# Kernel tuning notes

Measured on AMD Instinct MI355X. Metric: run time of the kernel, lower is better.

The kernel has to match this reference:

```python
import jax, jax.numpy as jnp
import numpy as np

N = 1024   # nnodes
H = 8      # attention heads
C = 32     # gnn_repr_size (per head)
HC = H * C # 256
E = 65536  # num edges
ER = 32    # edge_repr_size
F = 3      # feat_emb_size
NUM_STOPS = 512


def setup_inputs() -> dict:
    key = jax.random.key(0)
    ks = jax.random.split(key, 24)
    g = lambda i, shape, s: jax.random.normal(ks[i], shape, dtype=jnp.float32) * s
    return {
        "dist": jax.random.uniform(ks[0], (N, N), dtype=jnp.float32),
        "stops": jax.random.randint(ks[1], (NUM_STOPS,), 0, N),
        "weekday": 3,
        "vehicles": 5,
        "markov": jax.random.uniform(ks[2], (N, N), dtype=jnp.float32),
        "demand": jax.random.uniform(ks[3], (N, 1), dtype=jnp.float32),
        "capacity": 10,
        "edge_index": jax.random.randint(ks[4], (2, E), 0, N),
        # GATConv layer 1 (in=1, out=H*C, edge_dim=1)
        "W1": g(5, (1, HC), 1.0), "We1": g(6, (1, HC), 1.0),
        "a_src1": g(7, (H, C), 0.1), "a_dst1": g(8, (H, C), 0.1), "a_edge1": g(9, (H, C), 0.1),
        "b1": jnp.zeros((HC,), jnp.float32),
        # GATConv layer 2 (in=H*C, out=H*C)
        "W2": g(10, (HC, HC), 0.0625), "We2": g(11, (1, HC), 1.0),
        "a_src2": g(12, (H, C), 0.1), "a_dst2": g(13, (H, C), 0.1), "a_edge2": g(14, (H, C), 0.1),
        "b2": jnp.zeros((HC,), jnp.float32),
        # edge summarizer Linear(2*HC, ER)
        "Wes": g(15, (2 * HC, ER), 0.0442), "bes": jnp.zeros((ER,), jnp.float32),
        # scalar embeddings
        "emb_weekday": g(16, (7, F), 0.1), "emb_capacity": g(17, (26, F), 0.1), "emb_vehicle": g(18, (15, F), 0.1),
        # combiner MLP: Linear(N*ER + 3N + 3F, N), Linear(N, N)
        "Wc1": g(19, (N * ER + 3 * N + 3 * F, N), 0.0053), "bc1": jnp.zeros((N,), jnp.float32),
        "Wc2": g(20, (N, N), 0.03125), "bc2": jnp.zeros((N,), jnp.float32),
    }


def _gat(x, src, dst, edge_attr, W, We, a_src, a_dst, a_edge, b):
    """PyG GATConv (concat heads, eval mode so attention dropout is identity)."""
    h = (x @ W).reshape(-1, H, C)                   # [N, H, C]
    e = (edge_attr @ We).reshape(-1, H, C)          # [E, H, C]
    alpha = (h * a_src).sum(-1)[src] + (h * a_dst).sum(-1)[dst] + (e * a_edge).sum(-1)  # [E, H]
    alpha = jax.nn.leaky_relu(alpha, 0.2)
    # segment softmax over destination nodes
    m = jax.ops.segment_max(alpha, dst, num_segments=N)
    m = jnp.where(jnp.isfinite(m), m, 0.0)
    ex = jnp.exp(alpha - m[dst])
    denom = jax.ops.segment_sum(ex, dst, num_segments=N)
    coef = ex / (denom[dst] + 1e-16)                # [E, H]
    out = jax.ops.segment_sum(h[src] * coef[:, :, None], dst, num_segments=N)  # [N, H, C]
    return out.reshape(-1, HC) + b


def reference(dist, stops, weekday, vehicles, markov, demand, capacity, edge_index,
              W1, We1, a_src1, a_dst1, a_edge1, b1,
              W2, We2, a_src2, a_dst2, a_edge2, b2,
              Wes, bes, emb_weekday, emb_capacity, emb_vehicle,
              Wc1, bc1, Wc2, bc2):
    src, dst = edge_index[0], edge_index[1]
    dist = (dist - dist.min()) / (dist.max() - dist.min())
    edge_attr = markov[src, dst][:, None]           # [E, 1]
    x = _gat(demand, src, dst, edge_attr, W1, We1, a_src1, a_dst1, a_edge1, b1)
    x = jax.nn.relu(x)
    x = _gat(x, src, dst, edge_attr, W2, We2, a_src2, a_dst2, a_edge2, b2)
    x = jax.nn.relu(x)                              # [N, HC]
    # edge_summarizer(cat(x_i, x_j)) decomposed: x_i @ Wes_top + x_j @ Wes_bot + bes
    ea = x @ Wes[:HC]                               # [N, ER]
    eb = x @ Wes[HC:]                               # [N, ER]
    edge_repr = (ea[:, None, :] + eb[None, :, :] + bes).reshape(N, N * ER)
    wf = jnp.broadcast_to(emb_weekday[weekday][None, :], (N, F))
    cf = jnp.broadcast_to(emb_capacity[capacity][None, :], (N, F))
    vf = jnp.broadcast_to(emb_vehicle[vehicles][None, :], (N, F))
    sf = jnp.zeros((N,), jnp.float32).at[stops].set(1.0)
    sf = jnp.broadcast_to(sf[None, :], (N, N))
    combined = jnp.concatenate([edge_repr, dist, markov, wf, cf, vf, sf], axis=1)
    out = jax.nn.relu(combined @ Wc1 + bc1) @ Wc2 + bc2  # [N, N]
    return out
```

## Files before the change

### kernel.cpp

```cpp
#include <hip/hip_runtime.h>

#define NN 1024
#define NE 65536

typedef short v8s __attribute__((ext_vector_type(8)));
typedef float v4f __attribute__((ext_vector_type(4)));

constexpr size_t OF_SCAL = 0;
constexpr size_t OF_MMP  = 64;
constexpr size_t OF_DEG  = 1088;
constexpr size_t OF_OFF  = 2112;
constexpr size_t OF_CUR  = 3200;
constexpr size_t OF_EIDX = 4224;
constexpr size_t OF_MARK = 69760;
constexpr size_t OF_X1H  = 135296;
constexpr size_t OF_X1L  = 266368;
constexpr size_t OF_H2   = 397440;
constexpr size_t OF_S2S  = 659584;
constexpr size_t OF_S2D  = 667776;
constexpr size_t OF_DEN2 = 675968;
constexpr size_t OF_EX2  = 684160;
constexpr size_t OF_X2   = 1208448;
constexpr size_t OF_BCAT = 1470592;
constexpr size_t OF_EAB  = 1486976;
constexpr size_t OF_WVEC = 1552512;
constexpr size_t OF_SRP  = 1588608;
constexpr size_t OF_C0P  = 3685760;
constexpr size_t OF_SR   = 3759488;
constexpr size_t OF_BASE = 3792256;
constexpr size_t OF_AH   = 3793280;
constexpr size_t OF_AL   = 4858240;
constexpr size_t OF_BTH  = 5923200;
constexpr size_t OF_BTL  = 6988160;
constexpr size_t OF_HH   = 8053120;
constexpr size_t OF_HL   = 8577408;
constexpr size_t OF_W2TH = 9101696;
constexpr size_t OF_W2TL = 9134464;
constexpr size_t OF_WC2TH= 9167232;
constexpr size_t OF_WC2TL= 9691520;
constexpr size_t OF_P0   = 10215808;

__device__ inline unsigned short f2bf(float x){
  unsigned u = __float_as_uint(x);
  unsigned r = u + 0x7fffu + ((u>>16)&1u);
  return (unsigned short)(r>>16);
}
__device__ inline float bf2f(unsigned short h){
  return __uint_as_float(((unsigned)h)<<16);
}

__global__ void k_mm1(const float* __restrict__ dist, float* mnP, float* mxP, int* __restrict__ deg){
  __shared__ float smn[256], smx[256];
  int tid = threadIdx.x;
  if (blockIdx.x < 4) deg[blockIdx.x*256 + tid] = 0;
  float mn = 1e30f, mx = -1e30f;
  for (int i = blockIdx.x*256 + tid; i < NN*NN; i += gridDim.x*256){
    float v = dist[i]; mn = fminf(mn, v); mx = fmaxf(mx, v);
  }
  smn[tid]=mn; smx[tid]=mx; __syncthreads();
  for (int s=128; s>0; s>>=1){
    if (tid<s){ smn[tid]=fminf(smn[tid],smn[tid+s]); smx[tid]=fmaxf(smx[tid],smx[tid+s]); }
    __syncthreads();
  }
  if (tid==0){ mnP[blockIdx.x]=smn[0]; mxP[blockIdx.x]=smx[0]; }
}

__global__ __launch_bounds__(512) void k_misc(const float* mnP, const float* mxP, float* scal,
    const float* W1, const float* We1, const float* as1, const float* ad1, const float* ae1,
    const float* We2, const float* ae2,
    const float* ew, const float* ec, const float* ev,
    const int* wd, const int* cap, const int* veh, const int* stops, float* wvec,
    const float* Wes, float* Bcat){
  int b = blockIdx.x, t = threadIdx.x;
  if (b == 0){
    __shared__ float smn[512], smx[512];
    smn[t]=mnP[t]; smx[t]=mxP[t]; __syncthreads();
    for (int s=256; s>0; s>>=1){
      if (t<s){ smn[t]=fminf(smn[t],smn[t+s]); smx[t]=fmaxf(smx[t],smx[t+s]); }
      __syncthreads();
    }
    if (t==0){ scal[0]=smn[0]; scal[1]=1.0f/(smx[0]-smn[0]); }
  } else if (b == 1){
    if (t < 8){
      float s=0.f, d=0.f, e=0.f, e2=0.f;
      for (int c=0;c<32;c++){
        int i = t*32+c;
        s += W1[i]*as1[i]; d += W1[i]*ad1[i]; e += We1[i]*ae1[i]; e2 += We2[i]*ae2[i];
      }
      scal[16+t]=s; scal[24+t]=d; scal[32+t]=e; scal[40+t]=e2;
    }
  } else if (b == 2){
    for (int m = 32768 + t; m < 35904; m += 512){
      float v = 0.f;
      if (m >= 34816 && m < 34819) v = ew[wd[0]*3 + (m-34816)];
      else if (m >= 34819 && m < 34822) v = ec[cap[0]*3 + (m-34819)];
      else if (m >= 34822 && m < 34825) v = ev[veh[0]*3 + (m-34822)];
      wvec[m] = v;
    }
    __syncthreads();
    wvec[34825 + stops[t]] = 1.0f;
  } else {
    int idx = (b-3)*512 + t;
    int k = idx >> 6, r = idx & 63;
    Bcat[idx] = (r < 32) ? Wes[(size_t)k*32 + r] : Wes[(size_t)(256+k)*32 + (r-32)];
  }
}

__global__ void k_edges(const int* __restrict__ ei, const float* __restrict__ markov,
                        float* __restrict__ mark, int* __restrict__ deg){
  int e = blockIdx.x*256 + threadIdx.x;
  if (e >= NE) return;
  int s = ei[e], d = ei[NE+e];
  mark[e] = markov[(size_t)s*NN + d];
  atomicAdd(&deg[d], 1);
}

__global__ void k_scan(const int* deg, int* off, int* cur){
  __shared__ int tmp[NN];
  int t = threadIdx.x;
  tmp[t] = deg[t]; __syncthreads();
  for (int s=1; s<NN; s<<=1){
    int v = (t>=s) ? tmp[t-s] : 0;
    __syncthreads();
    tmp[t] += v;
    __syncthreads();
  }
  int ex = (t==0) ? 0 : tmp[t-1];
  off[t]=ex; cur[t]=ex;
  if (t==NN-1) off[NN]=tmp[NN-1];
}

__global__ void k_fill(const int* __restrict__ ei, int* __restrict__ cur, int* __restrict__ eidxl){
  int e = blockIdx.x*256 + threadIdx.x;
  if (e >= NE) return;
  int d = ei[NE+e];
  int p = atomicAdd(&cur[d], 1);
  eidxl[p] = e;
}

__global__ __launch_bounds__(64) void k_gat1x1(const int* __restrict__ ei, const int* __restrict__ eidxl,
    const int* __restrict__ off, const float* __restrict__ mark, const float* __restrict__ demand,
    const float* __restrict__ scal, const float* __restrict__ W1, const float* __restrict__ b1,
    unsigned short* __restrict__ X1h, unsigned short* __restrict__ X1l){
  int n = blockIdx.x, lane = threadIdx.x;
  int o0 = off[n], o1 = off[n+1];
  float dn = demand[n];
  float cs[8], cd[8], ce[8], mx[8];
  #pragma unroll
  for (int h=0;h<8;h++){ cs[h]=scal[16+h]; cd[h]=scal[24+h]; ce[h]=scal[32+h]; mx[h]=-1e30f; }
  for (int i=o0+lane; i<o1; i+=64){
    int e = eidxl[i]; float ds = demand[ei[e]]; float me = mark[e];
    #pragma unroll
    for (int h=0;h<8;h++){
      float a = ds*cs[h] + dn*cd[h] + me*ce[h];
      a = a < 0.f ? 0.2f*a : a;
      mx[h] = fmaxf(mx[h], a);
    }
  }
  #pragma unroll
  for (int s=32; s>0; s>>=1){
    #pragma unroll
    for (int h=0;h<8;h++) mx[h] = fmaxf(mx[h], __shfl_xor(mx[h], s));
  }
  float se[8], sd_[8];
  #pragma unroll
  for (int h=0;h<8;h++){ se[h]=0.f; sd_[h]=0.f; }
  for (int i=o0+lane; i<o1; i+=64){
    int e = eidxl[i]; float ds = demand[ei[e]]; float me = mark[e];
    #pragma unroll
    for (int h=0;h<8;h++){
      float a = ds*cs[h] + dn*cd[h] + me*ce[h];
      a = a < 0.f ? 0.2f*a : a;
      float ex = expf(a - mx[h]);
      se[h] += ex; sd_[h] += ex*ds;
    }
  }
  #pragma unroll
  for (int s=32; s>0; s>>=1){
    #pragma unroll
    for (int h=0;h<8;h++){ se[h] += __shfl_xor(se[h], s); sd_[h] += __shfl_xor(sd_[h], s); }
  }
  float t1v[8];
  #pragma unroll
  for (int h=0;h<8;h++) t1v[h] = sd_[h] / (se[h] + 1e-16f);
  #pragma unroll
  for (int q=0;q<4;q++){
    int hc = lane + q*64; int h = hc >> 5;
    float v = fmaxf(t1v[h]*W1[hc] + b1[hc], 0.f);
    unsigned short hh = f2bf(v);
    X1h[(size_t)n*256 + hc] = hh;
    X1l[(size_t)n*256 + hc] = f2bf(v - bf2f(hh));
  }
}

__global__ __launch_bounds__(256) void gemm64(const float* __restrict__ A, int lda,
    const float* __restrict__ B, int ldb, float* __restrict__ C, int ldc, int K,
    const float* __restrict__ bias, int dorelu){
  __shared__ float As[16][68];
  __shared__ float Bs[16][68];
  int tid = threadIdx.x;
  int tx = tid & 15, ty = tid >> 4;
  int row0 = ty*4, col0 = tx*4;
  int gm = blockIdx.y*64, gn = blockIdx.x*64;
  float acc[4][4] = {};
  for (int k0 = 0; k0 < K; k0 += 16){
    #pragma unroll
    for (int q=0;q<4;q++){
      int idx = tid*4+q; int i = idx>>4, kk = idx&15;
      As[kk][i] = A[(size_t)(gm+i)*lda + k0 + kk];
    }
    #pragma unroll
    for (int q=0;q<4;q++){
      int idx = tid*4+q; int kk = idx>>6, j = idx&63;
      Bs[kk][j] = B[(size_t)(k0+kk)*ldb + gn + j];
    }
    __syncthreads();
    #pragma unroll
    for (int kk=0;kk<16;kk++){
      float a0=As[kk][row0+0], a1=As[kk][row0+1], a2=As[kk][row0+2], a3=As[kk][row0+3];
      float b0=Bs[kk][col0+0], b1=Bs[kk][col0+1], b2=Bs[kk][col0+2], b3=Bs[kk][col0+3];
      acc[0][0]+=a0*b0; acc[0][1]+=a0*b1; acc[0][2]+=a0*b2; acc[0][3]+=a0*b3;
      acc[1][0]+=a1*b0; acc[1][1]+=a1*b1; acc[1][2]+=a1*b2; acc[1][3]+=a1*b3;
      acc[2][0]+=a2*b0; acc[2][1]+=a2*b1; acc[2][2]+=a2*b2; acc[2][3]+=a2*b3;
      acc[3][0]+=a3*b0; acc[3][1]+=a3*b1; acc[3][2]+=a3*b2; acc[3][3]+=a3*b3;
    }
    __syncthreads();
  }
  #pragma unroll
  for (int i=0;i<4;i++){
    #pragma unroll
    for (int j=0;j<4;j++){
      int cc = gn + col0 + j;
      float v = acc[i][j];
      if (bias) v += bias[cc];
      if (dorelu) v = fmaxf(v, 0.f);
      C[(size_t)(gm+row0+i)*ldc + cc] = v;
    }
  }
}

__global__ void k_s2(const float* __restrict__ h2, const float* __restrict__ as2,
                     const float* __restrict__ ad2, float* __restrict__ s2s, float* __restrict__ s2d){
  int idx = blockIdx.x*256 + threadIdx.x;
  if (idx >= NN*8) return;
  int n = idx >> 3, h = idx & 7;
  float ss = 0.f, sd = 0.f;
  for (int c=0;c<32;c++){
    float v = h2[(size_t)n*256 + h*32 + c];
    ss += v*as2[h*32+c]; sd += v*ad2[h*32+c];
  }
  s2s[idx]=ss; s2d[idx]=sd;
}

__global__ __launch_bounds__(64) void k_gat2maxex(const int* __restrict__ ei, const int* __restrict__ eidxl,
    const int* __restrict__ off, const float* __restrict__ mark, const float* __restrict__ s2s,
    const float* __restrict__ s2d, const float* __restrict__ scal,
    float* __restrict__ den, float* __restrict__ ex2){
  int n = blockIdx.x, lane = threadIdx.x;
  int o0 = off[n], o1 = off[n+1];
  float ce[8], sdn[8], mx[8];
  #pragma unroll
  for (int h=0;h<8;h++){ ce[h]=scal[40+h]; sdn[h]=s2d[n*8+h]; mx[h]=-1e30f; }
  for (int i=o0+lane; i<o1; i+=64){
    int e = eidxl[i]; int s = ei[e]; float me = mark[e];
    #pragma unroll
    for (int h=0;h<8;h++){
      float a = s2s[s*8+h] + sdn[h] + me*ce[h];
      a = a < 0.f ? 0.2f*a : a;
      mx[h] = fmaxf(mx[h], a);
    }
  }
  #pragma unroll
  for (int sft=32; sft>0; sft>>=1){
    #pragma unroll
    for (int h=0;h<8;h++) mx[h] = fmaxf(mx[h], __shfl_xor(mx[h], sft));
  }
  float se[8];
  #pragma unroll
  for (int h=0;h<8;h++) se[h]=0.f;
  for (int i=o0+lane; i<o1; i+=64){
    int e = eidxl[i]; int s = ei[e]; float me = mark[e];
    float exv[8];
    #pragma unroll
    for (int h=0;h<8;h++){
      float a = s2s[s*8+h] + sdn[h] + me*ce[h];
      a = a < 0.f ? 0.2f*a : a;
      exv[h] = expf(a - mx[h]);
      se[h] += exv[h];
    }
    #pragma unroll
    for (int h=0;h<8;h++) ex2[(size_t)e*8+h] = exv[h];
  }
  #pragma unroll
  for (int sft=32; sft>0; sft>>=1){
    #pragma unroll
    for (int h=0;h<8;h++) se[h] += __shfl_xor(se[h], sft);
  }
  if (lane==0){
    #pragma unroll
    for (int h=0;h<8;h++) den[n*8+h] = se[h];
  }
}

__global__ __launch_bounds__(256) void k_agg2(const int* __restrict__ ei, const int* __restrict__ eidxl,
    const int* __restrict__ off, const float* __restrict__ ex2, const float* __restrict__ den,
    const float* __restrict__ h2, const float* __restrict__ b2, float* __restrict__ x2){
  __shared__ int eL[64], sL[64];
  __shared__ float cf[64*8];
  int n = blockIdx.x, tid = threadIdx.x, h = tid >> 5;
  int o0 = off[n], o1 = off[n+1];
  float inv = 1.0f/(den[n*8+h] + 1e-16f);
  float acc = 0.f;
  for (int b = o0; b < o1; b += 64){
    int len = min(64, o1 - b);
    __syncthreads();
    if (tid < len){ int e = eidxl[b+tid]; eL[tid]=e; sL[tid]=ei[e]; }
    __syncthreads();
    for (int idx = tid; idx < len*8; idx += 256)
      cf[idx] = ex2[(size_t)eL[idx>>3]*8 + (idx&7)];
    __syncthreads();
    for (int j=0;j<len;j++){
      acc += cf[j*8 + h] * h2[(size_t)sL[j]*256 + tid];
    }
  }
  x2[(size_t)n*256 + tid] = fmaxf(acc*inv + b2[tid], 0.f);
}

__global__ void k_wvec(const float* __restrict__ eab, const float* __restrict__ bes,
                       float* __restrict__ wvec){
  int m = blockIdx.x*256 + threadIdx.x;
  int j = m >> 5, r = m & 31;
  wvec[m] = eab[(size_t)j*64 + 32 + r] + bes[r];
}

__global__ __launch_bounds__(256) void k_src0(const float* __restrict__ Wc1, const float* __restrict__ wvec,
                                              float* __restrict__ srP, float* __restrict__ c0P){
  __shared__ float c0s[256*4];
  int t = threadIdx.x;
  int kg = t & 31;
  int rg = t >> 5;
  int col = blockIdx.x*128 + kg*4;
  int chunk = blockIdx.y;
  int m0 = chunk*512;
  float sr[4][4];
  #pragma unroll
  for (int u=0;u<4;u++){ sr[u][0]=0.f; sr[u][1]=0.f; sr[u][2]=0.f; sr[u][3]=0.f; }
  float c0a[4] = {0.f,0.f,0.f,0.f};
  for (int jj=0; jj<16; ++jj){
    int rbase = m0 + jj*32 + rg*4;
    #pragma unroll
    for (int u=0;u<4;u++){
      int m = rbase + u;
      float4 w = make_float4(0.f,0.f,0.f,0.f);
      float wv = 0.f;
      if (m < 35849){
        w = *reinterpret_cast<const float4*>(&Wc1[(size_t)m*1024 + col]);
        wv = wvec[m];
      }
      c0a[0] += wv*w.x; c0a[1] += wv*w.y; c0a[2] += wv*w.z; c0a[3] += wv*w.w;
      if (chunk < 64){
        sr[u][0] += w.x; sr[u][1] += w.y; sr[u][2] += w.z; sr[u][3] += w.w;
      }
    }
  }
  if (chunk < 64){
    #pragma unroll
    for (int u=0;u<4;u++){
      int r = rg*4 + u;
      float4 v = make_float4(sr[u][0], sr[u][1], sr[u][2], sr[u][3]);
      *reinterpret_cast<float4*>(&srP[(size_t)(chunk*32 + r)*1024 + col]) = v;
    }
  }
  c0s[t*4+0]=c0a[0]; c0s[t*4+1]=c0a[1]; c0s[t*4+2]=c0a[2]; c0s[t*4+3]=c0a[3];
  __syncthreads();
  if (t < 32){
    float s0=0.f,s1=0.f,s2=0.f,s3=0.f;
    #pragma unroll
    for (int q=0;q<8;q++){
      int b = (t + q*32)*4;
      s0 += c0s[b+0]; s1 += c0s[b+1]; s2 += c0s[b+2]; s3 += c0s[b+3];
    }
    float4 v = make_float4(s0,s1,s2,s3);
    *reinterpret_cast<float4*>(&c0P[(size_t)chunk*1024 + blockIdx.x*128 + t*4]) = v;
  }
}

__global__ void k_stage2(const float* __restrict__ srP, const float* __restrict__ c0P,
                         const float* __restrict__ bc1, float* __restrict__ Sr, float* __restrict__ base){
  int idx = blockIdx.x*256 + threadIdx.x;
  if (idx < 8192){
    int r = idx >> 8, k4 = idx & 255;
    float s0=0.f,s1=0.f,s2=0.f,s3=0.f;
    for (int c=0;c<64;c++){
      float4 v = *reinterpret_cast<const float4*>(&srP[(size_t)(c*32 + r)*1024 + k4*4]);
      s0+=v.x; s1+=v.y; s2+=v.z; s3+=v.w;
    }
    float4 o = make_float4(s0,s1,s2,s3);
    *reinterpret_cast<float4*>(&Sr[(size_t)r*1024 + k4*4]) = o;
  } else if (idx < 8448){
    int k4 = idx - 8192;
    float4 b = *reinterpret_cast<const float4*>(&bc1[k4*4]);
    float s0=b.x, s1=b.y, s2=b.z, s3=b.w;
    for (int c=0;c<71;c++){
      float4 v = *reinterpret_cast<const float4*>(&c0P[(size_t)c*1024 + k4*4]);
      s0+=v.x; s1+=v.y; s2+=v.z; s3+=v.w;
    }
    float4 o = make_float4(s0,s1,s2,s3);
    *reinterpret_cast<float4*>(&base[k4*4]) = o;
  }
}

__global__ void k_cvtA(const float* __restrict__ dist, const float* __restrict__ markov,
                       const float* __restrict__ eab, const float* __restrict__ scal,
                       unsigned short* __restrict__ Ah, unsigned short* __restrict__ Al){
  int k = blockIdx.x*256 + threadIdx.x;
  int i = blockIdx.y;
  if (k >= 2080) return;
  float mn = scal[0], inv = scal[1];
  float v;
  if (k < 1024) v = (dist[(size_t)i*1024 + k] - mn)*inv;
  else if (k < 2048) v = markov[(size_t)i*1024 + (k-1024)];
  else v = eab[(size_t)i*64 + (k-2048)];
  unsigned short h = f2bf(v);
  Ah[(size_t)i*2080 + k] = h;
  Al[(size_t)i*2080 + k] = f2bf(v - bf2f(h));
}

__global__ void k_cvtT(const float* __restrict__ src, const float* __restrict__ src2, int k2,
                       int lds, int ldt, unsigned short* __restrict__ Th, unsigned short* __restrict__ Tl){
  __shared__ unsigned short shh[32][65], shl[32][65];
  int t = threadIdx.x;
  int k0 = blockIdx.x*32, n0 = blockIdx.y*64;
  #pragma unroll
  for (int q=0;q<8;q++){
    int idx = t + q*256;
    int kl = idx >> 6, nl = idx & 63;
    int k = k0 + kl;
    float v = (k < k2) ? src[(size_t)k*lds + n0 + nl] : src2[(size_t)(k-k2)*lds + n0 + nl];
    unsigned short h = f2bf(v);
    shh[kl][nl] = h;
    shl[kl][nl] = f2bf(v - bf2f(h));
  }
  __syncthreads();
  #pragma unroll
  for (int q=0;q<8;q++){
    int idx = t + q*256;
    int nl = idx >> 5, kl = idx & 31;
    Th[(size_t)(n0+nl)*ldt + k0 + kl] = shh[kl][nl];
    Tl[(size_t)(n0+nl)*ldt + k0 + kl] = shl[kl][nl];
  }
}

__global__ __launch_bounds__(256) void k_mfma128(
    const unsigned short* __restrict__ Ah, const unsigned short* __restrict__ Al, int lda,
    const unsigned short* __restrict__ Bth, const unsigned short* __restrict__ Btl, int ldb,
    float* __restrict__ Cp, int ldc, int kSteps, int kTot){
  __shared__ __align__(16) unsigned short Ash[128*32], Asl[128*32], Bsh[128*32], Bsl[128*32];
  int t = threadIdx.x;
  int wave = t >> 6, lane = t & 63;
  int wr = wave >> 1, wc = wave & 1;
  int gm = blockIdx.y*128, gn = blockIdx.x*128;
  float* plane = Cp + ((size_t)blockIdx.z << 20);
  int ks0 = blockIdx.z * kSteps;
  int ks1 = ks0 + kSteps; if (ks1 > kTot) ks1 = kTot;

  int kq = lane >> 4;
  int l15 = lane & 15;
  int r0s = t >> 2,        s0s = t & 3;
  int r1s = (t+256) >> 2,  s1s = t & 3;

  v4f acc[4][4];
  #pragma unroll
  for (int i=0;i<4;i++)
    #pragma unroll
    for (int j=0;j<4;j++) acc[i][j] = (v4f){0.f,0.f,0.f,0.f};

  for (int ks = ks0; ks < ks1; ++ks){
    int kb = ks*32;
    const size_t a0 = (size_t)(gm+r0s)*lda + kb + s0s*8;
    const size_t a1 = (size_t)(gm+r1s)*lda + kb + s1s*8;
    const size_t b0 = (size_t)(gn+r0s)*ldb + kb + s0s*8;
    const size_t b1 = (size_t)(gn+r1s)*ldb + kb + s1s*8;
    v8s gah0 = *(const v8s*)(Ah + a0), gah1 = *(const v8s*)(Ah + a1);
    v8s gal0 = *(const v8s*)(Al + a0), gal1 = *(const v8s*)(Al + a1);
    v8s gbh0 = *(const v8s*)(Bth + b0), gbh1 = *(const v8s*)(Bth + b1);
    v8s gbl0 = *(const v8s*)(Btl + b0), gbl1 = *(const v8s*)(Btl + b1);
    __syncthreads();
    int w0 = r0s*32 + ((s0s ^ ((r0s>>1)&3))*8);
    int w1 = r1s*32 + ((s1s ^ ((r1s>>1)&3))*8);
    *(v8s*)(Ash + w0) = gah0;  *(v8s*)(Ash + w1) = gah1;
    *(v8s*)(Asl + w0) = gal0;  *(v8s*)(Asl + w1) = gal1;
    *(v8s*)(Bsh + w0) = gbh0;  *(v8s*)(Bsh + w1) = gbh1;
    *(v8s*)(Bsl + w0) = gbl0;  *(v8s*)(Bsl + w1) = gbl1;
    __syncthreads();
    v8s fbh[4], fbl[4];
    #pragma unroll
    for (int fj=0; fj<4; fj++){
      int cb = wc*64 + fj*16 + l15;
      int boff = cb*32 + ((kq ^ ((cb>>1)&3))*8);
      fbh[fj] = *(v8s*)(Bsh + boff);
      fbl[fj] = *(v8s*)(Bsl + boff);
    }
    #pragma unroll
    for (int fi=0; fi<4; fi++){
      int ra = wr*64 + fi*16 + l15;
      int aoff = ra*32 + ((kq ^ ((ra>>1)&3))*8);
      v8s fah = *(v8s*)(Ash + aoff);
      v8s fal = *(v8s*)(Asl + aoff);
      #pragma unroll
      for (int fj=0; fj<4; fj++){
        acc[fi][fj] = __builtin_amdgcn_mfma_f32_16x16x32_bf16(fah, fbh[fj], acc[fi][fj], 0, 0, 0);
        acc[fi][fj] = __builtin_amdgcn_mfma_f32_16x16x32_bf16(fah, fbl[fj], acc[fi][fj], 0, 0, 0);
        acc[fi][fj] = __builtin_amdgcn_mfma_f32_16x16x32_bf16(fal, fbh[fj], acc[fi][fj], 0, 0, 0);
      }
    }
  }
  int row0 = gm + wr*64 + (lane>>4)*4;
  int col0 = gn + wc*64 + l15;
  #pragma unroll
  for (int fi=0; fi<4; fi++)
    #pragma unroll
    for (int fj=0; fj<4; fj++)
      #pragma unroll
      for (int r=0; r<4; r++)
        plane[(size_t)(row0 + fi*16 + r)*ldc + col0 + fj*16] = acc[fi][fj][r];
}

__global__ void k_fin2(const float* __restrict__ P, float* __restrict__ h2){
  int idx = blockIdx.x*256 + threadIdx.x;
  float4 a = *reinterpret_cast<const float4*>(P + (size_t)idx*4);
  float4 b = *reinterpret_cast<const float4*>(P + (1u<<20) + (size_t)idx*4);
  float4 o = make_float4(a.x+b.x, a.y+b.y, a.z+b.z, a.w+b.w);
  *reinterpret_cast<float4*>(h2 + (size_t)idx*4) = o;
}

__global__ void k_fin_hidden(const float* __restrict__ P, const float* __restrict__ base,
                             unsigned short* __restrict__ Hh, unsigned short* __restrict__ Hl){
  int idx = blockIdx.x*256 + threadIdx.x;
  float4 s = *reinterpret_cast<const float4*>(base + ((idx & 255)*4));
  #pragma unroll
  for (int p=0;p<8;p++){
    float4 v = *reinterpret_cast<const float4*>(P + ((size_t)p<<20) + (size_t)idx*4);
    s.x+=v.x; s.y+=v.y; s.z+=v.z; s.w+=v.w;
  }
  float vv[4] = {s.x, s.y, s.z, s.w};
  unsigned short hh[4], hl[4];
  #pragma unroll
  for (int q=0;q<4;q++){
    float x = fmaxf(vv[q], 0.f);
    hh[q] = f2bf(x);
    hl[q] = f2bf(x - bf2f(hh[q]));
  }
  *reinterpret_cast<uint2*>(Hh + (size_t)idx*4) = *reinterpret_cast<uint2*>(hh);
  *reinterpret_cast<uint2*>(Hl + (size_t)idx*4) = *reinterpret_cast<uint2*>(hl);
}

__global__ void k_fin_out(const float* __restrict__ P, const float* __restrict__ bc2,
                          float* __restrict__ out){
  int idx = blockIdx.x*256 + threadIdx.x;
  float4 s = *reinterpret_cast<const float4*>(bc2 + ((idx & 255)*4));
  #pragma unroll
  for (int p=0;p<8;p++){
    float4 v = *reinterpret_cast<const float4*>(P + ((size_t)p<<20) + (size_t)idx*4);
    s.x+=v.x; s.y+=v.y; s.z+=v.z; s.w+=v.w;
  }
  *reinterpret_cast<float4*>(out + (size_t)idx*4) = s;
}

extern "C" void kernel_launch(void* const* d_in, const int* in_sizes, int n_in,
                              void* d_out, int out_size, void* d_ws, size_t ws_size,
                              hipStream_t stream){
  const float* dist     = (const float*)d_in[0];
  const int*   stops    = (const int*)  d_in[1];
  const int*   weekday  = (const int*)  d_in[2];
  const int*   vehicles = (const int*)  d_in[3];
  const float* markov   = (const float*)d_in[4];
  const float* demand   = (const float*)d_in[5];
  const int*   capacity = (const int*)  d_in[6];
  const int*   ei       = (const int*)  d_in[7];
  const float* W1  = (const float*)d_in[8];
  const float* We1 = (const float*)d_in[9];
  const float* as1 = (const float*)d_in[10];
  const float* ad1 = (const float*)d_in[11];
  const float* ae1 = (const float*)d_in[12];
  const float* b1  = (const float*)d_in[13];
  const float* W2  = (const float*)d_in[14];
  const float* We2 = (const float*)d_in[15];
  const float* as2 = (const float*)d_in[16];
  const float* ad2 = (const float*)d_in[17];
  const float* ae2 = (const float*)d_in[18];
  const float* b2  = (const float*)d_in[19];
  const float* Wes = (const float*)d_in[20];
  const float* bes = (const float*)d_in[21];
  const float* ew  = (const float*)d_in[22];
  const float* ec  = (const float*)d_in[23];
  const float* ev  = (const float*)d_in[24];
  const float* Wc1 = (const float*)d_in[25];
  const float* bc1 = (const float*)d_in[26];
  const float* Wc2 = (const float*)d_in[27];
  const float* bc2 = (const float*)d_in[28];

  float* W    = (float*)d_ws;
  float* scal = W + OF_SCAL;
  float* mmP  = W + OF_MMP;
  int*   deg  = (int*)(W + OF_DEG);
  int*   off  = (int*)(W + OF_OFF);
  int*   cur  = (int*)(W + OF_CUR);
  int*   eidxl= (int*)(W + OF_EIDX);
  float* mark = W + OF_MARK;
  unsigned short* X1h = (unsigned short*)(W + OF_X1H);
  unsigned short* X1l = (unsigned short*)(W + OF_X1L);
  float* h2   = W + OF_H2;
  float* s2s  = W + OF_S2S;
  float* s2d  = W + OF_S2D;
  float* den2 = W + OF_DEN2;
  float* ex2  = W + OF_EX2;
  float* x2   = W + OF_X2;
  float* Bcat = W + OF_BCAT;
  float* eab  = W + OF_EAB;
  float* wvec = W + OF_WVEC;
  float* srP  = W + OF_SRP;
  float* c0P  = W + OF_C0P;
  float* Sr   = W + OF_SR;
  float* base = W + OF_BASE;
  unsigned short* Ah    = (unsigned short*)(W + OF_AH);
  unsigned short* Al    = (unsigned short*)(W + OF_AL);
  unsigned short* Bth   = (unsigned short*)(W + OF_BTH);
  unsigned short* Btl   = (unsigned short*)(W + OF_BTL);
  unsigned short* Hh    = (unsigned short*)(W + OF_HH);
  unsigned short* Hl    = (unsigned short*)(W + OF_HL);
  unsigned short* W2th  = (unsigned short*)(W + OF_W2TH);
  unsigned short* W2tl  = (unsigned short*)(W + OF_W2TL);
  unsigned short* Wc2th = (unsigned short*)(W + OF_WC2TH);
  unsigned short* Wc2tl = (unsigned short*)(W + OF_WC2TL);
  float* P0   = W + OF_P0;
  float* out  = (float*)d_out;

  k_mm1 <<<dim3(512), dim3(256), 0, stream>>>(dist, mmP, mmP+512, deg);
  k_misc<<<dim3(35), dim3(512), 0, stream>>>(mmP, mmP+512, scal, W1, We1, as1, ad1, ae1, We2, ae2,
                                             ew, ec, ev, weekday, capacity, vehicles, stops, wvec, Wes, Bcat);
  k_cvtT<<<dim3(8,4), dim3(256), 0, stream>>>(W2, W2, 1<<30, 256, 256, W2th, W2tl);
  k_cvtT<<<dim3(32,16), dim3(256), 0, stream>>>(Wc2, Wc2, 1<<30, 1024, 1024, Wc2th, Wc2tl);
  k_edges<<<dim3(256), dim3(256), 0, stream>>>(ei, markov, mark, deg);
  k_scan<<<dim3(1), dim3(1024), 0, stream>>>(deg, off, cur);
  k_fill<<<dim3(256), dim3(256), 0, stream>>>(ei, cur, eidxl);
  k_gat1x1<<<dim3(1024), dim3(64), 0, stream>>>(ei, eidxl, off, mark, demand, scal, W1, b1, X1h, X1l);
  k_mfma128<<<dim3(2,8,2), dim3(256), 0, stream>>>(X1h, X1l, 256, W2th, W2tl, 256, P0, 256, 4, 8);
  k_fin2<<<dim3(256), dim3(256), 0, stream>>>(P0, h2);
  k_s2  <<<dim3(32), dim3(256), 0, stream>>>(h2, as2, ad2, s2s, s2d);
  k_gat2maxex<<<dim3(1024), dim3(64), 0, stream>>>(ei, eidxl, off, mark, s2s, s2d, scal, den2, ex2);
  k_agg2<<<dim3(1024), dim3(256), 0, stream>>>(ei, eidxl, off, ex2, den2, h2, b2, x2);
  gemm64<<<dim3(1,16), dim3(256), 0, stream>>>(x2, 256, Bcat, 64, eab, 64, 256, (const float*)nullptr, 0);
  k_wvec<<<dim3(128), dim3(256), 0, stream>>>(eab, bes, wvec);
  k_src0<<<dim3(8,71), dim3(256), 0, stream>>>(Wc1, wvec, srP, c0P);
  k_stage2<<<dim3(33), dim3(256), 0, stream>>>(srP, c0P, bc1, Sr, base);
  k_cvtA<<<dim3(9,1024), dim3(256), 0, stream>>>(dist, markov, eab, scal, Ah, Al);
  k_cvtT<<<dim3(65,16), dim3(256), 0, stream>>>(Wc1 + (size_t)32768*1024, Sr, 2048, 1024, 2080, Bth, Btl);
  k_mfma128<<<dim3(8,8,8), dim3(256), 0, stream>>>(Ah, Al, 2080, Bth, Btl, 2080, P0, 1024, 9, 65);
  k_fin_hidden<<<dim3(1024), dim3(256), 0, stream>>>(P0, base, Hh, Hl);
  k_mfma128<<<dim3(8,8,8), dim3(256), 0, stream>>>(Hh, Hl, 1024, Wc2th, Wc2tl, 1024, P0, 1024, 4, 32);
  k_fin_out<<<dim3(1024), dim3(256), 0, stream>>>(P0, bc2, out);
}
```

Baseline: 201.0 us.

## Fuse small kernels and retune split-K partitioning across GEMM stages

Merges the two weight-transpose conversions into one launch, fuses the h2 split-K reduction with the per-head attention score computation, and folds the wvec bias add into the small gemm epilogue, removing several launches and round trips through global memory. It also doubles the chunk count in the Wc1 column-sum pass to expose more parallelism, and changes split-K factors: the W2 GEMM goes from 2 to 8 splits, while the large hidden and output GEMMs drop from 8 to 4 splits, with the matching reduce loops shortened. Workspace offsets are moved to fit the larger partial buffers. The trade-off is fewer parallel blocks in the big GEMMs against less partial-sum traffic.

```diff
diff --git a/kernel.cpp b/kernel.cpp
--- a/kernel.cpp
+++ b/kernel.cpp
@@ -25,20 +25,20 @@
 constexpr size_t OF_EAB  = 1486976;
 constexpr size_t OF_WVEC = 1552512;
 constexpr size_t OF_SRP  = 1588608;
-constexpr size_t OF_C0P  = 3685760;
-constexpr size_t OF_SR   = 3759488;
-constexpr size_t OF_BASE = 3792256;
-constexpr size_t OF_AH   = 3793280;
-constexpr size_t OF_AL   = 4858240;
-constexpr size_t OF_BTH  = 5923200;
-constexpr size_t OF_BTL  = 6988160;
-constexpr size_t OF_HH   = 8053120;
-constexpr size_t OF_HL   = 8577408;
-constexpr size_t OF_W2TH = 9101696;
-constexpr size_t OF_W2TL = 9134464;
-constexpr size_t OF_WC2TH= 9167232;
-constexpr size_t OF_WC2TL= 9691520;
-constexpr size_t OF_P0   = 10215808;
+constexpr size_t OF_C0P  = 5782912;
+constexpr size_t OF_SR   = 5928320;
+constexpr size_t OF_BASE = 5961088;
+constexpr size_t OF_AH   = 5962112;
+constexpr size_t OF_AL   = 7027072;
+constexpr size_t OF_BTH  = 8092032;
+constexpr size_t OF_BTL  = 9156992;
+constexpr size_t OF_HH   = 10221952;
+constexpr size_t OF_HL   = 10746240;
+constexpr size_t OF_W2TH = 11270528;
+constexpr size_t OF_W2TL = 11303296;
+constexpr size_t OF_WC2TH= 11336064;
+constexpr size_t OF_WC2TL= 11860352;
+constexpr size_t OF_P0   = 12384640;
 
 __device__ inline unsigned short f2bf(float x){
   unsigned u = __float_as_uint(x);
@@ -195,7 +195,7 @@
 
 __global__ __launch_bounds__(256) void gemm64(const float* __restrict__ A, int lda,
     const float* __restrict__ B, int ldb, float* __restrict__ C, int ldc, int K,
-    const float* __restrict__ bias, int dorelu){
+    float* __restrict__ wvec, const float* __restrict__ bes){
   __shared__ float As[16][68];
   __shared__ float Bs[16][68];
   int tid = threadIdx.x;
@@ -232,24 +232,32 @@
     for (int j=0;j<4;j++){
       int cc = gn + col0 + j;
       float v = acc[i][j];
-      if (bias) v += bias[cc];
-      if (dorelu) v = fmaxf(v, 0.f);
       C[(size_t)(gm+row0+i)*ldc + cc] = v;
-    }
-  }
-}
-
-__global__ void k_s2(const float* __restrict__ h2, const float* __restrict__ as2,
-                     const float* __restrict__ ad2, float* __restrict__ s2s, float* __restrict__ s2d){
-  int idx = blockIdx.x*256 + threadIdx.x;
-  if (idx >= NN*8) return;
-  int n = idx >> 3, h = idx & 7;
-  float ss = 0.f, sd = 0.f;
-  for (int c=0;c<32;c++){
-    float v = h2[(size_t)n*256 + h*32 + c];
-    ss += v*as2[h*32+c]; sd += v*ad2[h*32+c];
-  }
-  s2s[idx]=ss; s2d[idx]=sd;
+      if (wvec && cc >= 32){
+        wvec[(size_t)(gm+row0+i)*32 + (cc-32)] = v + bes[cc-32];
+      }
+    }
+  }
+}
+
+__global__ __launch_bounds__(64) void k_fin2s2(const float* __restrict__ P,
+    const float* __restrict__ as2, const float* __restrict__ ad2,
+    float* __restrict__ h2, float* __restrict__ s2s, float* __restrict__ s2d){
+  int n = blockIdx.x, l = threadIdx.x;
+  size_t off = (size_t)n*256 + l*4;
+  float4 s = make_float4(0.f,0.f,0.f,0.f);
+  #pragma unroll
+  for (int p=0;p<8;p++){
+    float4 v = *reinterpret_cast<const float4*>(P + ((size_t)p<<20) + off);
+    s.x+=v.x; s.y+=v.y; s.z+=v.z; s.w+=v.w;
+  }
+  *reinterpret_cast<float4*>(h2 + off) = s;
+  int c = l*4;
+  float ss = s.x*as2[c]+s.y*as2[c+1]+s.z*as2[c+2]+s.w*as2[c+3];
+  float sd = s.x*ad2[c]+s.y*ad2[c+1]+s.z*ad2[c+2]+s.w*ad2[c+3];
+  #pragma unroll
+  for (int sft=1; sft<8; sft<<=1){ ss += __shfl_xor(ss, sft); sd += __shfl_xor(sd, sft); }
+  if ((l&7)==0){ s2s[n*8 + (l>>3)] = ss; s2d[n*8 + (l>>3)] = sd; }
 }
 
 __global__ __launch_bounds__(64) void k_gat2maxex(const int* __restrict__ ei, const int* __restrict__ eidxl,
@@ -326,13 +334,6 @@
   x2[(size_t)n*256 + tid] = fmaxf(acc*inv + b2[tid], 0.f);
 }
 
-__global__ void k_wvec(const float* __restrict__ eab, const float* __restrict__ bes,
-                       float* __restrict__ wvec){
-  int m = blockIdx.x*256 + threadIdx.x;
-  int j = m >> 5, r = m & 31;
-  wvec[m] = eab[(size_t)j*64 + 32 + r] + bes[r];
-}
-
 __global__ __launch_bounds__(256) void k_src0(const float* __restrict__ Wc1, const float* __restrict__ wvec,
                                               float* __restrict__ srP, float* __restrict__ c0P){
   __shared__ float c0s[256*4];
@@ -341,12 +342,12 @@
   int rg = t >> 5;
   int col = blockIdx.x*128 + kg*4;
   int chunk = blockIdx.y;
-  int m0 = chunk*512;
+  int m0 = chunk*256;
   float sr[4][4];
   #pragma unroll
   for (int u=0;u<4;u++){ sr[u][0]=0.f; sr[u][1]=0.f; sr[u][2]=0.f; sr[u][3]=0.f; }
   float c0a[4] = {0.f,0.f,0.f,0.f};
-  for (int jj=0; jj<16; ++jj){
+  for (int jj=0; jj<8; ++jj){
     int rbase = m0 + jj*32 + rg*4;
     #pragma unroll
     for (int u=0;u<4;u++){
@@ -358,12 +359,12 @@
         wv = wvec[m];
       }
       c0a[0] += wv*w.x; c0a[1] += wv*w.y; c0a[2] += wv*w.z; c0a[3] += wv*w.w;
-      if (chunk < 64){
+      if (chunk < 128){
         sr[u][0] += w.x; sr[u][1] += w.y; sr[u][2] += w.z; sr[u][3] += w.w;
       }
     }
   }
-  if (chunk < 64){
+  if (chunk < 128){
     #pragma unroll
     for (int u=0;u<4;u++){
       int r = rg*4 + u;
@@ -391,7 +392,7 @@
   if (idx < 8192){
     int r = idx >> 8, k4 = idx & 255;
     float s0=0.f,s1=0.f,s2=0.f,s3=0.f;
-    for (int c=0;c<64;c++){
+    for (int c=0;c<128;c++){
       float4 v = *reinterpret_cast<const float4*>(&srP[(size_t)(c*32 + r)*1024 + k4*4]);
       s0+=v.x; s1+=v.y; s2+=v.z; s3+=v.w;
     }
@@ -401,7 +402,7 @@
     int k4 = idx - 8192;
     float4 b = *reinterpret_cast<const float4*>(&bc1[k4*4]);
     float s0=b.x, s1=b.y, s2=b.z, s3=b.w;
-    for (int c=0;c<71;c++){
+    for (int c=0;c<141;c++){
       float4 v = *reinterpret_cast<const float4*>(&c0P[(size_t)c*1024 + k4*4]);
       s0+=v.x; s1+=v.y; s2+=v.z; s3+=v.w;
     }
@@ -426,11 +427,10 @@
   Al[(size_t)i*2080 + k] = f2bf(v - bf2f(h));
 }
 
-__global__ void k_cvtT(const float* __restrict__ src, const float* __restrict__ src2, int k2,
-                       int lds, int ldt, unsigned short* __restrict__ Th, unsigned short* __restrict__ Tl){
+__device__ inline void cvtT_body(const float* __restrict__ src, const float* __restrict__ src2, int k2,
+    int lds, int ldt, unsigned short* __restrict__ Th, unsigned short* __restrict__ Tl,
+    int k0, int n0, int t){
   __shared__ unsigned short shh[32][65], shl[32][65];
-  int t = threadIdx.x;
-  int k0 = blockIdx.x*32, n0 = blockIdx.y*64;
   #pragma unroll
   for (int q=0;q<8;q++){
     int idx = t + q*256;
@@ -448,6 +448,23 @@
     int nl = idx >> 5, kl = idx & 31;
     Th[(size_t)(n0+nl)*ldt + k0 + kl] = shh[kl][nl];
     Tl[(size_t)(n0+nl)*ldt + k0 + kl] = shl[kl][nl];
+  }
+}
+
+__global__ void k_cvtT(const float* __restrict__ src, const float* __restrict__ src2, int k2,
+                       int lds, int ldt, unsigned short* __restrict__ Th, unsigned short* __restrict__ Tl){
+  cvtT_body(src, src2, k2, lds, ldt, Th, Tl, blockIdx.x*32, blockIdx.y*64, threadIdx.x);
+}
+
+__global__ void k_cvtW(const float* __restrict__ W2, const float* __restrict__ Wc2,
+                       unsigned short* __restrict__ W2th, unsigned short* __restrict__ W2tl,
+                       unsigned short* __restrict__ Wc2th, unsigned short* __restrict__ Wc2tl){
+  int bx = blockIdx.x, by = blockIdx.y;
+  if (by < 16){
+    cvtT_body(Wc2, Wc2, 1<<30, 1024, 1024, Wc2th, Wc2tl, bx*32, by*64, threadIdx.x);
+  } else {
+    if (bx >= 8) return;
+    cvtT_body(W2, W2, 1<<30, 256, 256, W2th, W2tl, bx*32, (by-16)*64, threadIdx.x);
   }
 }
 
@@ -526,20 +543,12 @@
         plane[(size_t)(row0 + fi*16 + r)*ldc + col0 + fj*16] = acc[fi][fj][r];
 }
 
-__global__ void k_fin2(const float* __restrict__ P, float* __restrict__ h2){
-  int idx = blockIdx.x*256 + threadIdx.x;
-  float4 a = *reinterpret_cast<const float4*>(P + (size_t)idx*4);
-  float4 b = *reinterpret_cast<const float4*>(P + (1u<<20) + (size_t)idx*4);
-  float4 o = make_float4(a.x+b.x, a.y+b.y, a.z+b.z, a.w+b.w);
-  *reinterpret_cast<float4*>(h2 + (size_t)idx*4) = o;
-}
-
 __global__ void k_fin_hidden(const float* __restrict__ P, const float* __restrict__ base,
                              unsigned short* __restrict__ Hh, unsigned short* __restrict__ Hl){
   int idx = blockIdx.x*256 + threadIdx.x;
   float4 s = *reinterpret_cast<const float4*>(base + ((idx & 255)*4));
   #pragma unroll
-  for (int p=0;p<8;p++){
+  for (int p=0;p<4;p++){
     float4 v = *reinterpret_cast<const float4*>(P + ((size_t)p<<20) + (size_t)idx*4);
     s.x+=v.x; s.y+=v.y; s.z+=v.z; s.w+=v.w;
   }
@@ -560,7 +569,7 @@
   int idx = blockIdx.x*256 + threadIdx.x;
   float4 s = *reinterpret_cast<const float4*>(bc2 + ((idx & 255)*4));
   #pragma unroll
-  for (int p=0;p<8;p++){
+  for (int p=0;p<4;p++){
     float4 v = *reinterpret_cast<const float4*>(P + ((size_t)p<<20) + (size_t)idx*4);
     s.x+=v.x; s.y+=v.y; s.z+=v.z; s.w+=v.w;
   }
@@ -639,25 +648,22 @@
   k_mm1 <<<dim3(512), dim3(256), 0, stream>>>(dist, mmP, mmP+512, deg);
   k_misc<<<dim3(35), dim3(512), 0, stream>>>(mmP, mmP+512, scal, W1, We1, as1, ad1, ae1, We2, ae2,
                                              ew, ec, ev, weekday, capacity, vehicles, stops, wvec, Wes, Bcat);
-  k_cvtT<<<dim3(8,4), dim3(256), 0, stream>>>(W2, W2, 1<<30, 256, 256, W2th, W2tl);
-  k_cvtT<<<dim3(32,16), dim3(256), 0, stream>>>(Wc2, Wc2, 1<<30, 1024, 1024, Wc2th, Wc2tl);
+  k_cvtW<<<dim3(32,20), dim3(256), 0, stream>>>(W2, Wc2, W2th, W2tl, Wc2th, Wc2tl);
   k_edges<<<dim3(256), dim3(256), 0, stream>>>(ei, markov, mark, deg);
   k_scan<<<dim3(1), dim3(1024), 0, stream>>>(deg, off, cur);
   k_fill<<<dim3(256), dim3(256), 0, stream>>>(ei, cur, eidxl);
   k_gat1x1<<<dim3(1024), dim3(64), 0, stream>>>(ei, eidxl, off, mark, demand, scal, W1, b1, X1h, X1l);
-  k_mfma128<<<dim3(2,8,2), dim3(256), 0, stream>>>(X1h, X1l, 256, W2th, W2tl, 256, P0, 256, 4, 8);
-  k_fin2<<<dim3(256), dim3(256), 0, stream>>>(P0, h2);
-  k_s2  <<<dim3(32), dim3(256), 0, stream>>>(h2, as2, ad2, s2s, s2d);
+  k_mfma128<<<dim3(2,8,8), dim3(256), 0, stream>>>(X1h, X1l, 256, W2th, W2tl, 256, P0, 256, 1, 8);
+  k_fin2s2<<<dim3(1024), dim3(64), 0, stream>>>(P0, as2, ad2, h2, s2s, s2d);
   k_gat2maxex<<<dim3(1024), dim3(64), 0, stream>>>(ei, eidxl, off, mark, s2s, s2d, scal, den2, ex2);
   k_agg2<<<dim3(1024), dim3(256), 0, stream>>>(ei, eidxl, off, ex2, den2, h2, b2, x2);
-  gemm64<<<dim3(1,16), dim3(256), 0, stream>>>(x2, 256, Bcat, 64, eab, 64, 256, (const float*)nullptr, 0);
-  k_wvec<<<dim3(128), dim3(256), 0, stream>>>(eab, bes, wvec);
-  k_src0<<<dim3(8,71), dim3(256), 0, stream>>>(Wc1, wvec, srP, c0P);
+  gemm64<<<dim3(1,16), dim3(256), 0, stream>>>(x2, 256, Bcat, 64, eab, 64, 256, wvec, bes);
+  k_src0<<<dim3(8,141), dim3(256), 0, stream>>>(Wc1, wvec, srP, c0P);
   k_stage2<<<dim3(33), dim3(256), 0, stream>>>(srP, c0P, bc1, Sr, base);
   k_cvtA<<<dim3(9,1024), dim3(256), 0, stream>>>(dist, markov, eab, scal, Ah, Al);
   k_cvtT<<<dim3(65,16), dim3(256), 0, stream>>>(Wc1 + (size_t)32768*1024, Sr, 2048, 1024, 2080, Bth, Btl);
-  k_mfma128<<<dim3(8,8,8), dim3(256), 0, stream>>>(Ah, Al, 2080, Bth, Btl, 2080, P0, 1024, 9, 65);
+  k_mfma128<<<dim3(8,8,4), dim3(256), 0, stream>>>(Ah, Al, 2080, Bth, Btl, 2080, P0, 1024, 17, 65);
   k_fin_hidden<<<dim3(1024), dim3(256), 0, stream>>>(P0, base, Hh, Hl);
-  k_mfma128<<<dim3(8,8,8), dim3(256), 0, stream>>>(Hh, Hl, 1024, Wc2th, Wc2tl, 1024, P0, 1024, 4, 32);
+  k_mfma128<<<dim3(8,8,4), dim3(256), 0, stream>>>(Hh, Hl, 1024, Wc2th, Wc2tl, 1024, P0, 1024, 8, 32);
   k_fin_out<<<dim3(1024), dim3(256), 0, stream>>>(P0, bc2, out);
 }
```

New measurement: 211.5 us. 5.2% more time.
